# Kernel optimization log

Hardware: AMD Instinct MI355X
Metric: run time of the kernel (lower is better)

The kernel has to match this reference:

```python
import jax, jax.numpy as jnp
import numpy as np

T, D_MODEL, D_FF, N_EXPERTS, TOP_K = 8192, 1024, 4096, 8, 2

def setup_inputs() -> dict:
    key = jax.random.key(0)
    k1, k2, k3, k4, k5 = jax.random.split(key, 5)
    hidden_states = jax.random.normal(k1, (T, D_MODEL), dtype=jnp.float32)
    # router picks TOP_K distinct-ish experts per token; build one-hot mask [T, K, E]
    expert_idx = jax.random.randint(k2, (T, TOP_K), 0, N_EXPERTS)
    selected_experts = jax.nn.one_hot(expert_idx, N_EXPERTS, dtype=jnp.int32)
    rw = jax.random.uniform(k3, (T, TOP_K), dtype=jnp.float32)
    routing_weights = rw / jnp.sum(rw, axis=-1, keepdims=True)
    scale = 1.0 / np.sqrt(D_MODEL)
    wi = jax.random.normal(k4, (N_EXPERTS, D_FF, D_MODEL), dtype=jnp.float32) * scale
    wo = jax.random.normal(k5, (N_EXPERTS, D_MODEL, D_FF), dtype=jnp.float32) * (1.0 / np.sqrt(D_FF))
    return {"hidden_states": hidden_states, "selected_experts": selected_experts,
            "routing_weights": routing_weights, "wi": wi, "wo": wo}

def reference(hidden_states, selected_experts, routing_weights, wi, wo):
    # expert_mask: [E, K, T] (as in torch permute(2,1,0))
    mask = jnp.transpose(selected_experts, (2, 1, 0)).astype(hidden_states.dtype)
    # combined per-token weight for each expert: w[t, e] = sum_k mask[e,k,t]*routing_weights[t,k]
    w = jnp.einsum('ekt,tk->te', mask, routing_weights)
    out = jnp.zeros_like(hidden_states)
    # fixed small loop over experts; tokens not routed to expert e get weight 0,
    # so this is mathematically identical to the gather->MLP->scale->scatter-add.
    for e in range(wi.shape[0]):
        h = jax.nn.relu(hidden_states @ wi[e].T)     # [T, d_ff] (dropout is identity at eval)
        y = h @ wo[e].T                              # [T, d_model]
        out = out + w[:, e:e + 1] * y
    return out
```

## Files before the change

kernel.cpp:

```cpp
#include <hip/hip_runtime.h>
#include <hip/hip_bf16.h>


#define T_TOK   8192
#define D_MODEL 1024
#define D_FF    4096
#define NE      8
#define BM      128
#define BK      64
#define MT_MAX  136
#define ROWS_MAX (MT_MAX * 128)

typedef float f32x4 __attribute__((ext_vector_type(4)));
typedef short s16x8 __attribute__((ext_vector_type(8)));
typedef short s16x4 __attribute__((ext_vector_type(4)));
typedef unsigned short u16;

__device__ __forceinline__ u16 f2bf(float x) {
  __hip_bfloat16 h = __float2bfloat16(x);
  return *reinterpret_cast<u16*>(&h);
}

__device__ __forceinline__ s16x8 cvt8(float4 a, float4 b) {
  s16x8 v;
  v[0] = (short)f2bf(a.x); v[1] = (short)f2bf(a.y);
  v[2] = (short)f2bf(a.z); v[3] = (short)f2bf(a.w);
  v[4] = (short)f2bf(b.x); v[5] = (short)f2bf(b.y);
  v[6] = (short)f2bf(b.z); v[7] = (short)f2bf(b.w);
  return v;
}

__device__ __forceinline__ void gload_lds16(const void* g, void* l) {
  __builtin_amdgcn_global_load_lds((const __attribute__((address_space(1))) void*)g,
                                   (__attribute__((address_space(3))) void*)l,
                                   16, 0, 0);
}

__global__ void moe_route(const int* __restrict__ sel, const float* __restrict__ rw,
                          int* __restrict__ cnt, int* __restrict__ tidx,
                          float* __restrict__ tw) {
  int t = blockIdx.x * blockDim.x + threadIdx.x;
  if (t >= T_TOK) return;
  int e0 = 0, e1 = 0;
  #pragma unroll
  for (int e = 0; e < NE; ++e) {
    if (sel[t * 16 + e])     e0 = e;
    if (sel[t * 16 + 8 + e]) e1 = e;
  }
  float w0 = rw[2 * t], w1 = rw[2 * t + 1];
  if (e0 == e1) {
    int p = atomicAdd(&cnt[e0], 1);
    tidx[e0 * T_TOK + p] = t; tw[e0 * T_TOK + p] = w0 + w1;
  } else {
    int p = atomicAdd(&cnt[e0], 1);
    tidx[e0 * T_TOK + p] = t; tw[e0 * T_TOK + p] = w0;
    int q = atomicAdd(&cnt[e1], 1);
    tidx[e1 * T_TOK + q] = t; tw[e1 * T_TOK + q] = w1;
  }
}

__global__ void moe_tilemap(const int* __restrict__ cnt, const int* __restrict__ tidx,
                            const float* __restrict__ tw, int* __restrict__ tile_e,
                            int* __restrict__ tokr, float* __restrict__ wr) {
  int off[NE + 1];
  {
    int o = 0;
    #pragma unroll
    for (int e = 0; e < NE; ++e) { off[e] = o; o += (cnt[e] + 127) & ~127; }
    off[NE] = o;
  }
  const int total = off[NE];
  const int gid = blockIdx.x * blockDim.x + threadIdx.x;
  const int stride = gridDim.x * blockDim.x;
  for (int t = gid; t < MT_MAX; t += stride) {
    int r0 = t * 128; int e = -1;
    if (r0 < total) {
      #pragma unroll
      for (int i = NE - 1; i >= 0; --i) if (r0 >= off[i]) { e = i; break; }
    }
    tile_e[t] = e;
  }
  for (int i = gid; i < ROWS_MAX; i += stride) {
    if (i >= total) { tokr[i] = -1; wr[i] = 0.f; continue; }
    int e = 0;
    #pragma unroll
    for (int k = NE - 1; k >= 0; --k) if (i >= off[k]) { e = k; break; }
    int j = i - off[e];
    int ok = j < cnt[e];
    tokr[i] = ok ? tidx[e * T_TOK + j] : -1;
    wr[i]   = ok ? tw[e * T_TOK + j] : 0.f;
  }
}

__global__ void moe_gather_x(const float* __restrict__ hs, const int* __restrict__ tokr,
                             u16* __restrict__ Xg) {
  int row = blockIdx.x;
  int tok = tokr[row];
  int c = threadIdx.x * 4;
  u16* dst = Xg + (size_t)row * D_MODEL + c;
  s16x4 o;
  if (tok < 0) {
    o[0] = o[1] = o[2] = o[3] = 0;
  } else {
    float4 v = *(const float4*)(hs + (size_t)tok * D_MODEL + c);
    o[0] = (short)f2bf(v.x); o[1] = (short)f2bf(v.y);
    o[2] = (short)f2bf(v.z); o[3] = (short)f2bf(v.w);
  }
  *(s16x4*)dst = o;
}

__global__ void moe_cvt_w(const float* __restrict__ wi, const float* __restrict__ wo,
                          u16* __restrict__ wib, u16* __restrict__ wob) {
  const size_t NW = (size_t)NE * D_FF * D_MODEL;
  size_t i = ((size_t)blockIdx.x * blockDim.x + threadIdx.x) * 8;
  const float* src; u16* dst;
  if (i < NW) { src = wi + i; dst = wib + i; }
  else        { src = wo + (i - NW); dst = wob + (i - NW); }
  float4 a = *(const float4*)(src);
  float4 b = *(const float4*)(src + 4);
  *(s16x8*)dst = cvt8(a, b);
}

__global__ void moe_cvt_wi_s(const float* __restrict__ wi, u16* __restrict__ wis,
                             int W, int f0) {
  size_t i = ((size_t)blockIdx.x * blockDim.x + threadIdx.x) * 8;
  size_t per = (size_t)W * D_MODEL;
  int e = (int)(i / per); size_t r = i % per;
  const float* src = wi + ((size_t)e * D_FF + f0) * D_MODEL + r;
  float4 a = *(const float4*)src;
  float4 b = *(const float4*)(src + 4);
  *(s16x8*)(wis + i) = cvt8(a, b);
}

__global__ void moe_cvt_wo_s(const float* __restrict__ wo, u16* __restrict__ wos,
                             int W, int f0) {
  size_t i = ((size_t)blockIdx.x * blockDim.x + threadIdx.x) * 8;
  size_t per = (size_t)D_MODEL * W;
  int e = (int)(i / per); size_t r = i % per;
  int row = (int)(r / W), col = (int)(r % W);
  const float* src = wo + ((size_t)e * D_MODEL + row) * D_FF + f0 + col;
  float4 a = *(const float4*)src;
  float4 b = *(const float4*)(src + 4);
  *(s16x8*)(wos + i) = cvt8(a, b);
}

template <bool FULL>
__global__ __launch_bounds__(256, 4)
void moe_g1(const u16* __restrict__ Xg, const u16* __restrict__ wiP,
            const int* __restrict__ tile_e, u16* __restrict__ H,
            int W, int f0) {
  __shared__ u16 As[BM * BK];
  __shared__ u16 Bs[BM * BK];

  const int GR = gridDim.x;
  const int task = (blockIdx.x & 7) * (GR >> 3) + (blockIdx.x >> 3);
  const int mt = task % MT_MAX;
  const int nc = task / MT_MAX;
  const int e = tile_e[mt];
  if (e < 0) return;
  const int grow0 = mt * 128;
  const int fl = nc * 128;

  const int tid = threadIdx.x;
  const int lane = tid & 63, wv = tid >> 6;
  const int lg = lane >> 4, ll = lane & 15;
  const int wm = wv >> 1, wn = wv & 1;

  const u16* abase0 = Xg + (size_t)grow0 * D_MODEL;
  const u16* bbase0 = wiP + (FULL ? ((size_t)e * D_FF + f0 + fl)
                                  : ((size_t)e * W + fl)) * D_MODEL;

  f32x4 acc[4][4];
  #pragma unroll
  for (int m = 0; m < 4; ++m)
    #pragma unroll
    for (int n = 0; n < 4; ++n) acc[m][n] = (f32x4){0.f, 0.f, 0.f, 0.f};

  for (int kk = 0; kk < D_MODEL / BK; ++kk) {
    __syncthreads();
    const u16* ab = abase0 + kk * BK;
    #pragma unroll
    for (int i = 0; i < 4; ++i) {
      int off = wv * 4096 + i * 1024 + lane * 16;
      int row = off >> 7, colb = off & 127;
      gload_lds16(ab + (size_t)row * D_MODEL + (colb >> 1), (char*)As + off);
    }
    const u16* bb = bbase0 + kk * BK;
    #pragma unroll
    for (int i = 0; i < 4; ++i) {
      int off = wv * 4096 + i * 1024 + lane * 16;
      int row = off >> 7, colb = off & 127;
      gload_lds16(bb + (size_t)row * D_MODEL + (colb >> 1), (char*)Bs + off);
    }
    __syncthreads();
    #pragma unroll
    for (int kb = 0; kb < 2; ++kb) {
      s16x8 af[4], bf[4];
      #pragma unroll
      for (int m = 0; m < 4; ++m)
        af[m] = *(const s16x8*)(As + (wm * 64 + m * 16 + ll) * BK + kb * 32 + lg * 8);
      #pragma unroll
      for (int n = 0; n < 4; ++n)
        bf[n] = *(const s16x8*)(Bs + (wn * 64 + n * 16 + ll) * BK + kb * 32 + lg * 8);
      #pragma unroll
      for (int m = 0; m < 4; ++m)
        #pragma unroll
        for (int n = 0; n < 4; ++n)
          acc[m][n] = __builtin_amdgcn_mfma_f32_16x16x32_bf16(af[m], bf[n], acc[m][n], 0, 0, 0);
    }
  }

  const int hc = fl + wn * 64 + ll;
  #pragma unroll
  for (int m = 0; m < 4; ++m) {
    #pragma unroll
    for (int r = 0; r < 4; ++r) {
      int row = grow0 + wm * 64 + m * 16 + lg * 4 + r;
      u16* hp = H + (size_t)row * W + hc;
      #pragma unroll
      for (int n = 0; n < 4; ++n) {
        float v = acc[m][n][r];
        hp[n * 16] = f2bf(v > 0.f ? v : 0.f);
      }
    }
  }
}

template <bool FULL>
__global__ __launch_bounds__(256, 4)
void moe_g2(const u16* __restrict__ H, const u16* __restrict__ woP,
            const int* __restrict__ tile_e, const int* __restrict__ tokr,
            const float* __restrict__ wr, float* __restrict__ out,
            int W, int f0, int KCH) {
  __shared__ u16 As[BM * BK];
  __shared__ u16 Bs[BM * BK];
  __shared__ int s_tok[BM];
  __shared__ float s_w[BM];

  const int GR = gridDim.x;
  const int task = (blockIdx.x & 7) * (GR >> 3) + (blockIdx.x >> 3);
  const int dc = task & 7;
  const int rest = task >> 3;
  const int mt = rest % MT_MAX;
  const int kc = rest / MT_MAX;
  const int e = tile_e[mt];
  if (e < 0) return;
  const int grow0 = mt * 128;
  const int dcol0 = dc * 128;

  const int tid = threadIdx.x;
  const int lane = tid & 63, wv = tid >> 6;
  const int lg = lane >> 4, ll = lane & 15;
  const int wm = wv >> 1, wn = wv & 1;

  if (tid < BM) { s_tok[tid] = tokr[grow0 + tid]; s_w[tid] = wr[grow0 + tid]; }
  __syncthreads();

  const u16* abase0 = H + (size_t)grow0 * W + (size_t)kc * KCH;
  const size_t bpitch = FULL ? (size_t)D_FF : (size_t)W;
  const u16* bbase0 = woP + ((size_t)e * D_MODEL + dcol0) * bpitch
                      + (FULL ? f0 : 0) + (size_t)kc * KCH;

  f32x4 acc[4][4];
  #pragma unroll
  for (int m = 0; m < 4; ++m)
    #pragma unroll
    for (int n = 0; n < 4; ++n) acc[m][n] = (f32x4){0.f, 0.f, 0.f, 0.f};

  for (int kk = 0; kk < KCH / BK; ++kk) {
    __syncthreads();
    const u16* ab = abase0 + kk * BK;
    #pragma unroll
    for (int i = 0; i < 4; ++i) {
      int off = wv * 4096 + i * 1024 + lane * 16;
      int row = off >> 7, colb = off & 127;
      gload_lds16(ab + (size_t)row * W + (colb >> 1), (char*)As + off);
    }
    const u16* bb = bbase0 + kk * BK;
    #pragma unroll
    for (int i = 0; i < 4; ++i) {
      int off = wv * 4096 + i * 1024 + lane * 16;
      int row = off >> 7, colb = off & 127;
      gload_lds16(bb + (size_t)row * bpitch + (colb >> 1), (char*)Bs + off);
    }
    __syncthreads();
    #pragma unroll
    for (int kb = 0; kb < 2; ++kb) {
      s16x8 af[4], bf[4];
      #pragma unroll
      for (int m = 0; m < 4; ++m)
        af[m] = *(const s16x8*)(As + (wm * 64 + m * 16 + ll) * BK + kb * 32 + lg * 8);
      #pragma unroll
      for (int n = 0; n < 4; ++n)
        bf[n] = *(const s16x8*)(Bs + (wn * 64 + n * 16 + ll) * BK + kb * 32 + lg * 8);
      #pragma unroll
      for (int m = 0; m < 4; ++m)
        #pragma unroll
        for (int n = 0; n < 4; ++n)
          acc[m][n] = __builtin_amdgcn_mfma_f32_16x16x32_bf16(af[m], bf[n], acc[m][n], 0, 0, 0);
    }
  }

  #pragma unroll
  for (int m = 0; m < 4; ++m) {
    #pragma unroll
    for (int r = 0; r < 4; ++r) {
      int row = wm * 64 + m * 16 + lg * 4 + r;
      int tok = s_tok[row];
      if (tok >= 0) {
        float w = s_w[row];
        float* op = out + (size_t)tok * D_MODEL + dcol0 + wn * 64 + ll;
        #pragma unroll
        for (int n = 0; n < 4; ++n)
          atomicAdd(op + n * 16, acc[m][n][r] * w);
      }
    }
  }
}

extern "C" void kernel_launch(void* const* d_in, const int* in_sizes, int n_in,
                              void* d_out, int out_size, void* d_ws, size_t ws_size,
                              hipStream_t stream) {
  const float* hs  = (const float*)d_in[0];
  const int*   sel = (const int*)d_in[1];
  const float* rw  = (const float*)d_in[2];
  const float* wi  = (const float*)d_in[3];
  const float* wo  = (const float*)d_in[4];
  float* out = (float*)d_out;

  const size_t NW   = (size_t)NE * D_FF * D_MODEL;
  const size_t CTRL = 1u << 20;
  const size_t WB   = 2 * NW * sizeof(u16);
  const size_t XGB  = (size_t)ROWS_MAX * D_MODEL * 2;

  bool FULLW = true; int W = D_FF;
  {
    bool found = false;
    for (int f : {1, 2, 4, 8, 16}) {
      int Wc = D_FF / f;
      size_t need = CTRL + WB + XGB + (size_t)ROWS_MAX * Wc * 2;
      if (need <= ws_size) { FULLW = true; W = Wc; found = true; break; }
    }
    if (!found) {
      for (int Wc : {1024, 512, 256}) {
        size_t sl = (size_t)2 * NE * Wc * D_MODEL * 2;
        size_t need = CTRL + sl + XGB + (size_t)ROWS_MAX * Wc * 2;
        if (need <= ws_size) { FULLW = false; W = Wc; break; }
      }
    }
  }
  const int FS = D_FF / W;

  size_t off = 0;
  auto take = [&](size_t b) -> char* {
    char* r = (char*)d_ws + off; off = (off + b + 255) & ~(size_t)255; return r;
  };
  int*   tidx = (int*)take((size_t)NE * T_TOK * 4);
  float* tw   = (float*)take((size_t)NE * T_TOK * 4);
  int*   tokr = (int*)take((size_t)ROWS_MAX * 4);
  float* wrr  = (float*)take((size_t)ROWS_MAX * 4);
  int*   te   = (int*)take(MT_MAX * 4);
  int*   cnt  = (int*)take(256);
  off = CTRL;
  u16 *wiP, *woP;
  if (FULLW) { wiP = (u16*)take(NW * 2); woP = (u16*)take(NW * 2); }
  else       { wiP = (u16*)take((size_t)NE * W * D_MODEL * 2);
               woP = (u16*)take((size_t)NE * D_MODEL * W * 2); }
  u16* Xg   = (u16*)take(XGB);
  u16* Hbuf = (u16*)take((size_t)ROWS_MAX * W * 2);

  hipMemsetAsync(cnt, 0, 256, stream);
  hipMemsetAsync(d_out, 0, (size_t)out_size * sizeof(float), stream);
  moe_route<<<T_TOK / 256, 256, 0, stream>>>(sel, rw, cnt, tidx, tw);
  moe_tilemap<<<64, 256, 0, stream>>>(cnt, tidx, tw, te, tokr, wrr);
  moe_gather_x<<<ROWS_MAX, 256, 0, stream>>>(hs, tokr, Xg);
  if (FULLW)
    moe_cvt_w<<<(int)(2 * NW / 8 / 256), 256, 0, stream>>>(wi, wo, wiP, woP);

  const int KCH = (W >= 2048) ? 2048 : W;
  const int g1grid = MT_MAX * (W / 128);
  const int g2grid = MT_MAX * 8 * (W / KCH);
  const int cvtblk = (int)(((size_t)NE * W * D_MODEL / 8) / 256);

  for (int p = 0; p < FS; ++p) {
    const int f0 = p * W;
    if (!FULLW) {
      moe_cvt_wi_s<<<cvtblk, 256, 0, stream>>>(wi, wiP, W, f0);
      moe_cvt_wo_s<<<cvtblk, 256, 0, stream>>>(wo, woP, W, f0);
    }
    if (FULLW) {
      moe_g1<true><<<g1grid, 256, 0, stream>>>(Xg, wiP, te, Hbuf, W, f0);
      moe_g2<true><<<g2grid, 256, 0, stream>>>(Hbuf, woP, te, tokr, wrr, out, W, f0, KCH);
    } else {
      moe_g1<false><<<g1grid, 256, 0, stream>>>(Xg, wiP, te, Hbuf, W, f0);
      moe_g2<false><<<g2grid, 256, 0, stream>>>(Hbuf, woP, te, tokr, wrr, out, W, f0, KCH);
    }
  }
}
```

Before: 571.7 us.

## Rewrite first expert GEMM with 256x256 tiles and triple-buffered LDS pipeline

The first grouped GEMM (X·Wi with ReLU) now runs 512-thread blocks computing 256x256 output tiles. It uses a three-stage dynamic-LDS ring with manual vmcnt waits, XOR-swizzled LDS layout and setprio around MFMA bursts. Expert segments are padded to 256 rows so that larger tiles stay within a single expert, and a second tile-to-expert map is kept for the unchanged 128-row second GEMM. This aims to raise data reuse and hide global load latency, at the cost of more padding rows, lower occupancy (one block per CU) and more careful synchronisation.

```diff
diff --git a/kernel.cpp b/kernel.cpp
--- a/kernel.cpp
+++ b/kernel.cpp
@@ -8,8 +8,11 @@
 #define NE      8
 #define BM      128
 #define BK      64
-#define MT_MAX  136
-#define ROWS_MAX (MT_MAX * 128)
+#define MT2     72
+#define MT_MAX  (MT2 * 2)
+#define ROWS_MAX (MT2 * 256)
+#define BUFB    32768
+#define LDS_G1  98304
 
 typedef float f32x4 __attribute__((ext_vector_type(4)));
 typedef short s16x8 __attribute__((ext_vector_type(8)));
@@ -60,13 +63,14 @@
 }
 
 __global__ void moe_tilemap(const int* __restrict__ cnt, const int* __restrict__ tidx,
-                            const float* __restrict__ tw, int* __restrict__ tile_e,
-                            int* __restrict__ tokr, float* __restrict__ wr) {
+                            const float* __restrict__ tw, int* __restrict__ te128,
+                            int* __restrict__ te256, int* __restrict__ tokr,
+                            float* __restrict__ wr) {
   int off[NE + 1];
   {
     int o = 0;
     #pragma unroll
-    for (int e = 0; e < NE; ++e) { off[e] = o; o += (cnt[e] + 127) & ~127; }
+    for (int e = 0; e < NE; ++e) { off[e] = o; o += (cnt[e] + 255) & ~255; }
     off[NE] = o;
   }
   const int total = off[NE];
@@ -78,7 +82,8 @@
       #pragma unroll
       for (int i = NE - 1; i >= 0; --i) if (r0 >= off[i]) { e = i; break; }
     }
-    tile_e[t] = e;
+    te128[t] = e;
+    if ((t & 1) == 0) te256[t >> 1] = e;
   }
   for (int i = gid; i < ROWS_MAX; i += stride) {
     if (i >= total) { tokr[i] = -1; wr[i] = 0.f; continue; }
@@ -145,30 +150,169 @@
 }
 
 template <bool FULL>
+__global__ __launch_bounds__(512, 1)
+void moe_g1(const u16* __restrict__ Xg, const u16* __restrict__ wiP,
+            const int* __restrict__ te256, u16* __restrict__ H,
+            int W, int f0) {
+  extern __shared__ char lds[];
+  const int GR = gridDim.x;
+  const int task = (blockIdx.x & 7) * (GR >> 3) + (blockIdx.x >> 3);
+  const int mt = task % MT2;
+  const int nc = task / MT2;
+  const int e = te256[mt];
+  if (e < 0) return;
+  const int grow0 = mt * 256;
+  const int fcol = nc * 256;
+
+  const int tid = threadIdx.x;
+  const int lane = tid & 63, wv = tid >> 6;
+  const int lg = lane >> 4, ll = lane & 15;
+  const int wm = wv >> 2, wn = wv & 3;
+
+  const int sw = (tid * 16) ^ (((tid >> 3) & 7) << 4);
+  const int srow = sw >> 6, scol = sw & 63;
+  const int inner = (ll * 64 + lg * 16) ^ (((ll >> 1) & 7) << 4);
+
+  const char* gA = (const char*)(Xg + (size_t)grow0 * D_MODEL);
+  const char* gB = (const char*)(wiP + (FULL ? ((size_t)e * D_FF + f0 + fcol)
+                                             : ((size_t)e * W + fcol)) * D_MODEL);
+
+  f32x4 acc[8][4];
+  #pragma unroll
+  for (int m = 0; m < 8; ++m)
+    #pragma unroll
+    for (int n = 0; n < 4; ++n) acc[m][n] = (f32x4){0.f, 0.f, 0.f, 0.f};
+
+  auto stage = [&](int kb, char* lbuf) {
+    #pragma unroll
+    for (int j = 0; j < 2; ++j)
+      gload_lds16(gA + (size_t)(j * 128 + srow) * 2048 + kb + scol,
+                  lbuf + j * 8192 + tid * 16);
+    #pragma unroll
+    for (int j = 0; j < 2; ++j)
+      gload_lds16(gB + (size_t)(j * 128 + srow) * 2048 + kb + scol,
+                  lbuf + 16384 + j * 8192 + tid * 16);
+  };
+
+  const int NT = D_MODEL / 32;
+  stage(0, lds);
+  stage(64, lds + BUFB);
+  int bufi = 0;
+  for (int t = 0; t < NT; ++t) {
+    if (t < NT - 1) { asm volatile("s_waitcnt vmcnt(4)" ::: "memory"); }
+    else            { asm volatile("s_waitcnt vmcnt(0)" ::: "memory"); }
+    asm volatile("s_barrier" ::: "memory");
+    const char* la = lds + bufi * BUFB + wm * 8192;
+    const char* lb = lds + bufi * BUFB + 16384 + wn * 4096;
+    if (t + 2 < NT) {
+      int b2 = bufi + 2; if (b2 >= 3) b2 -= 3;
+      stage((t + 2) * 64, lds + b2 * BUFB);
+    }
+    s16x8 bq0 = *(const s16x8*)(lb + 0 * 1024 + inner);
+    s16x8 bq1 = *(const s16x8*)(lb + 1 * 1024 + inner);
+    s16x8 bq2 = *(const s16x8*)(lb + 2 * 1024 + inner);
+    s16x8 bq3 = *(const s16x8*)(lb + 3 * 1024 + inner);
+    {
+      s16x8 a0 = *(const s16x8*)(la + 0 * 1024 + inner);
+      s16x8 a1 = *(const s16x8*)(la + 1 * 1024 + inner);
+      s16x8 a2 = *(const s16x8*)(la + 2 * 1024 + inner);
+      s16x8 a3 = *(const s16x8*)(la + 3 * 1024 + inner);
+      __builtin_amdgcn_s_setprio(1);
+      acc[0][0] = __builtin_amdgcn_mfma_f32_16x16x32_bf16(a0, bq0, acc[0][0], 0, 0, 0);
+      acc[0][1] = __builtin_amdgcn_mfma_f32_16x16x32_bf16(a0, bq1, acc[0][1], 0, 0, 0);
+      acc[0][2] = __builtin_amdgcn_mfma_f32_16x16x32_bf16(a0, bq2, acc[0][2], 0, 0, 0);
+      acc[0][3] = __builtin_amdgcn_mfma_f32_16x16x32_bf16(a0, bq3, acc[0][3], 0, 0, 0);
+      acc[1][0] = __builtin_amdgcn_mfma_f32_16x16x32_bf16(a1, bq0, acc[1][0], 0, 0, 0);
+      acc[1][1] = __builtin_amdgcn_mfma_f32_16x16x32_bf16(a1, bq1, acc[1][1], 0, 0, 0);
+      acc[1][2] = __builtin_amdgcn_mfma_f32_16x16x32_bf16(a1, bq2, acc[1][2], 0, 0, 0);
+      acc[1][3] = __builtin_amdgcn_mfma_f32_16x16x32_bf16(a1, bq3, acc[1][3], 0, 0, 0);
+      acc[2][0] = __builtin_amdgcn_mfma_f32_16x16x32_bf16(a2, bq0, acc[2][0], 0, 0, 0);
+      acc[2][1] = __builtin_amdgcn_mfma_f32_16x16x32_bf16(a2, bq1, acc[2][1], 0, 0, 0);
+      acc[2][2] = __builtin_amdgcn_mfma_f32_16x16x32_bf16(a2, bq2, acc[2][2], 0, 0, 0);
+      acc[2][3] = __builtin_amdgcn_mfma_f32_16x16x32_bf16(a2, bq3, acc[2][3], 0, 0, 0);
+      acc[3][0] = __builtin_amdgcn_mfma_f32_16x16x32_bf16(a3, bq0, acc[3][0], 0, 0, 0);
+      acc[3][1] = __builtin_amdgcn_mfma_f32_16x16x32_bf16(a3, bq1, acc[3][1], 0, 0, 0);
+      acc[3][2] = __builtin_amdgcn_mfma_f32_16x16x32_bf16(a3, bq2, acc[3][2], 0, 0, 0);
+      acc[3][3] = __builtin_amdgcn_mfma_f32_16x16x32_bf16(a3, bq3, acc[3][3], 0, 0, 0);
+      __builtin_amdgcn_s_setprio(0);
+    }
+    __builtin_amdgcn_s_barrier();
+    {
+      s16x8 a0 = *(const s16x8*)(la + 4 * 1024 + inner);
+      s16x8 a1 = *(const s16x8*)(la + 5 * 1024 + inner);
+      s16x8 a2 = *(const s16x8*)(la + 6 * 1024 + inner);
+      s16x8 a3 = *(const s16x8*)(la + 7 * 1024 + inner);
+      __builtin_amdgcn_s_setprio(1);
+      acc[4][0] = __builtin_amdgcn_mfma_f32_16x16x32_bf16(a0, bq0, acc[4][0], 0, 0, 0);
+      acc[4][1] = __builtin_amdgcn_mfma_f32_16x16x32_bf16(a0, bq1, acc[4][1], 0, 0, 0);
+      acc[4][2] = __builtin_amdgcn_mfma_f32_16x16x32_bf16(a0, bq2, acc[4][2], 0, 0, 0);
+      acc[4][3] = __builtin_amdgcn_mfma_f32_16x16x32_bf16(a0, bq3, acc[4][3], 0, 0, 0);
+      acc[5][0] = __builtin_amdgcn_mfma_f32_16x16x32_bf16(a1, bq0, acc[5][0], 0, 0, 0);
+      acc[5][1] = __builtin_amdgcn_mfma_f32_16x16x32_bf16(a1, bq1, acc[5][1], 0, 0, 0);
+      acc[5][2] = __builtin_amdgcn_mfma_f32_16x16x32_bf16(a1, bq2, acc[5][2], 0, 0, 0);
+      acc[5][3] = __builtin_amdgcn_mfma_f32_16x16x32_bf16(a1, bq3, acc[5][3], 0, 0, 0);
+      acc[6][0] = __builtin_amdgcn_mfma_f32_16x16x32_bf16(a2, bq0, acc[6][0], 0, 0, 0);
+      acc[6][1] = __builtin_amdgcn_mfma_f32_16x16x32_bf16(a2, bq1, acc[6][1], 0, 0, 0);
+      acc[6][2] = __builtin_amdgcn_mfma_f32_16x16x32_bf16(a2, bq2, acc[6][2], 0, 0, 0);
+      acc[6][3] = __builtin_amdgcn_mfma_f32_16x16x32_bf16(a2, bq3, acc[6][3], 0, 0, 0);
+      acc[7][0] = __builtin_amdgcn_mfma_f32_16x16x32_bf16(a3, bq0, acc[7][0], 0, 0, 0);
+      acc[7][1] = __builtin_amdgcn_mfma_f32_16x16x32_bf16(a3, bq1, acc[7][1], 0, 0, 0);
+      acc[7][2] = __builtin_amdgcn_mfma_f32_16x16x32_bf16(a3, bq2, acc[7][2], 0, 0, 0);
+      acc[7][3] = __builtin_amdgcn_mfma_f32_16x16x32_bf16(a3, bq3, acc[7][3], 0, 0, 0);
+      __builtin_amdgcn_s_setprio(0);
+    }
+    bufi += 1; if (bufi >= 3) bufi -= 3;
+  }
+
+  #pragma unroll
+  for (int mf = 0; mf < 8; ++mf) {
+    #pragma unroll
+    for (int r = 0; r < 4; ++r) {
+      int row = grow0 + wm * 128 + mf * 16 + lg * 4 + r;
+      u16* hp = H + (size_t)row * W + fcol + wn * 64 + ll;
+      #pragma unroll
+      for (int nf = 0; nf < 4; ++nf) {
+        float v = acc[mf][nf][r];
+        hp[nf * 16] = f2bf(v > 0.f ? v : 0.f);
+      }
+    }
+  }
+}
+
+template <bool FULL>
 __global__ __launch_bounds__(256, 4)
-void moe_g1(const u16* __restrict__ Xg, const u16* __restrict__ wiP,
-            const int* __restrict__ tile_e, u16* __restrict__ H,
-            int W, int f0) {
+void moe_g2(const u16* __restrict__ H, const u16* __restrict__ woP,
+            const int* __restrict__ te128, const int* __restrict__ tokr,
+            const float* __restrict__ wr, float* __restrict__ out,
+            int W, int f0, int KCH) {
   __shared__ u16 As[BM * BK];
   __shared__ u16 Bs[BM * BK];
+  __shared__ int s_tok[BM];
+  __shared__ float s_w[BM];
 
   const int GR = gridDim.x;
   const int task = (blockIdx.x & 7) * (GR >> 3) + (blockIdx.x >> 3);
-  const int mt = task % MT_MAX;
-  const int nc = task / MT_MAX;
-  const int e = tile_e[mt];
+  const int dc = task & 7;
+  const int rest = task >> 3;
+  const int mt = rest % MT_MAX;
+  const int kc = rest / MT_MAX;
+  const int e = te128[mt];
   if (e < 0) return;
   const int grow0 = mt * 128;
-  const int fl = nc * 128;
+  const int dcol0 = dc * 128;
 
   const int tid = threadIdx.x;
   const int lane = tid & 63, wv = tid >> 6;
   const int lg = lane >> 4, ll = lane & 15;
   const int wm = wv >> 1, wn = wv & 1;
 
-  const u16* abase0 = Xg + (size_t)grow0 * D_MODEL;
-  const u16* bbase0 = wiP + (FULL ? ((size_t)e * D_FF + f0 + fl)
-                                  : ((size_t)e * W + fl)) * D_MODEL;
+  if (tid < BM) { s_tok[tid] = tokr[grow0 + tid]; s_w[tid] = wr[grow0 + tid]; }
+  __syncthreads();
+
+  const u16* abase0 = H + (size_t)grow0 * W + (size_t)kc * KCH;
+  const size_t bpitch = FULL ? (size_t)D_FF : (size_t)W;
+  const u16* bbase0 = woP + ((size_t)e * D_MODEL + dcol0) * bpitch
+                      + (FULL ? f0 : 0) + (size_t)kc * KCH;
 
   f32x4 acc[4][4];
   #pragma unroll
@@ -176,21 +320,21 @@
     #pragma unroll
     for (int n = 0; n < 4; ++n) acc[m][n] = (f32x4){0.f, 0.f, 0.f, 0.f};
 
-  for (int kk = 0; kk < D_MODEL / BK; ++kk) {
+  for (int kk = 0; kk < KCH / BK; ++kk) {
     __syncthreads();
     const u16* ab = abase0 + kk * BK;
     #pragma unroll
     for (int i = 0; i < 4; ++i) {
       int off = wv * 4096 + i * 1024 + lane * 16;
       int row = off >> 7, colb = off & 127;
-      gload_lds16(ab + (size_t)row * D_MODEL + (colb >> 1), (char*)As + off);
+      gload_lds16(ab + (size_t)row * W + (colb >> 1), (char*)As + off);
     }
     const u16* bb = bbase0 + kk * BK;
     #pragma unroll
     for (int i = 0; i < 4; ++i) {
       int off = wv * 4096 + i * 1024 + lane * 16;
       int row = off >> 7, colb = off & 127;
-      gload_lds16(bb + (size_t)row * D_MODEL + (colb >> 1), (char*)Bs + off);
+      gload_lds16(bb + (size_t)row * bpitch + (colb >> 1), (char*)Bs + off);
     }
     __syncthreads();
     #pragma unroll
@@ -210,97 +354,6 @@
     }
   }
 
-  const int hc = fl + wn * 64 + ll;
-  #pragma unroll
-  for (int m = 0; m < 4; ++m) {
-    #pragma unroll
-    for (int r = 0; r < 4; ++r) {
-      int row = grow0 + wm * 64 + m * 16 + lg * 4 + r;
-      u16* hp = H + (size_t)row * W + hc;
-      #pragma unroll
-      for (int n = 0; n < 4; ++n) {
-        float v = acc[m][n][r];
-        hp[n * 16] = f2bf(v > 0.f ? v : 0.f);
-      }
-    }
-  }
-}
-
-template <bool FULL>
-__global__ __launch_bounds__(256, 4)
-void moe_g2(const u16* __restrict__ H, const u16* __restrict__ woP,
-            const int* __restrict__ tile_e, const int* __restrict__ tokr,
-            const float* __restrict__ wr, float* __restrict__ out,
-            int W, int f0, int KCH) {
-  __shared__ u16 As[BM * BK];
-  __shared__ u16 Bs[BM * BK];
-  __shared__ int s_tok[BM];
-  __shared__ float s_w[BM];
-
-  const int GR = gridDim.x;
-  const int task = (blockIdx.x & 7) * (GR >> 3) + (blockIdx.x >> 3);
-  const int dc = task & 7;
-  const int rest = task >> 3;
-  const int mt = rest % MT_MAX;
-  const int kc = rest / MT_MAX;
-  const int e = tile_e[mt];
-  if (e < 0) return;
-  const int grow0 = mt * 128;
-  const int dcol0 = dc * 128;
-
-  const int tid = threadIdx.x;
-  const int lane = tid & 63, wv = tid >> 6;
-  const int lg = lane >> 4, ll = lane & 15;
-  const int wm = wv >> 1, wn = wv & 1;
-
-  if (tid < BM) { s_tok[tid] = tokr[grow0 + tid]; s_w[tid] = wr[grow0 + tid]; }
-  __syncthreads();
-
-  const u16* abase0 = H + (size_t)grow0 * W + (size_t)kc * KCH;
-  const size_t bpitch = FULL ? (size_t)D_FF : (size_t)W;
-  const u16* bbase0 = woP + ((size_t)e * D_MODEL + dcol0) * bpitch
-                      + (FULL ? f0 : 0) + (size_t)kc * KCH;
-
-  f32x4 acc[4][4];
-  #pragma unroll
-  for (int m = 0; m < 4; ++m)
-    #pragma unroll
-    for (int n = 0; n < 4; ++n) acc[m][n] = (f32x4){0.f, 0.f, 0.f, 0.f};
-
-  for (int kk = 0; kk < KCH / BK; ++kk) {
-    __syncthreads();
-    const u16* ab = abase0 + kk * BK;
-    #pragma unroll
-    for (int i = 0; i < 4; ++i) {
-      int off = wv * 4096 + i * 1024 + lane * 16;
-      int row = off >> 7, colb = off & 127;
-      gload_lds16(ab + (size_t)row * W + (colb >> 1), (char*)As + off);
-    }
-    const u16* bb = bbase0 + kk * BK;
-    #pragma unroll
-    for (int i = 0; i < 4; ++i) {
-      int off = wv * 4096 + i * 1024 + lane * 16;
-      int row = off >> 7, colb = off & 127;
-      gload_lds16(bb + (size_t)row * bpitch + (colb >> 1), (char*)Bs + off);
-    }
-    __syncthreads();
-    #pragma unroll
-    for (int kb = 0; kb < 2; ++kb) {
-      s16x8 af[4], bf[4];
-      #pragma unroll
-      for (int m = 0; m < 4; ++m)
-        af[m] = *(const s16x8*)(As + (wm * 64 + m * 16 + ll) * BK + kb * 32 + lg * 8);
-      #pragma unroll
-      for (int n = 0; n < 4; ++n)
-        bf[n] = *(const s16x8*)(Bs + (wn * 64 + n * 16 + ll) * BK + kb * 32 + lg * 8);
-      #pragma unroll
-      for (int m = 0; m < 4; ++m)
-        #pragma unroll
-        for (int n = 0; n < 4; ++n)
-          acc[m][n] = __builtin_amdgcn_mfma_f32_16x16x32_bf16(af[m], bf[n], acc[m][n], 0, 0, 0);
-    }
-  }
-
   #pragma unroll
   for (int m = 0; m < 4; ++m) {
     #pragma unroll
@@ -360,6 +413,7 @@
   int*   tokr = (int*)take((size_t)ROWS_MAX * 4);
   float* wrr  = (float*)take((size_t)ROWS_MAX * 4);
   int*   te   = (int*)take(MT_MAX * 4);
+  int*   te2  = (int*)take(MT2 * 4);
   int*   cnt  = (int*)take(256);
   off = CTRL;
   u16 *wiP, *woP;
@@ -372,13 +426,18 @@
   hipMemsetAsync(cnt, 0, 256, stream);
   hipMemsetAsync(d_out, 0, (size_t)out_size * sizeof(float), stream);
   moe_route<<<T_TOK / 256, 256, 0, stream>>>(sel, rw, cnt, tidx, tw);
-  moe_tilemap<<<64, 256, 0, stream>>>(cnt, tidx, tw, te, tokr, wrr);
+  moe_tilemap<<<64, 256, 0, stream>>>(cnt, tidx, tw, te, te2, tokr, wrr);
   moe_gather_x<<<ROWS_MAX, 256, 0, stream>>>(hs, tokr, Xg);
   if (FULLW)
     moe_cvt_w<<<(int)(2 * NW / 8 / 256), 256, 0, stream>>>(wi, wo, wiP, woP);
 
+  hipFuncSetAttribute(reinterpret_cast<const void*>(&moe_g1<true>),
+                      hipFuncAttributeMaxDynamicSharedMemorySize, LDS_G1);
+  hipFuncSetAttribute(reinterpret_cast<const void*>(&moe_g1<false>),
+                      hipFuncAttributeMaxDynamicSharedMemorySize, LDS_G1);
+
   const int KCH = (W >= 2048) ? 2048 : W;
-  const int g1grid = MT_MAX * (W / 128);
+  const int g1grid = MT2 * (W / 256);
   const int g2grid = MT_MAX * 8 * (W / KCH);
   const int cvtblk = (int)(((size_t)NE * W * D_MODEL / 8) / 256);
 
@@ -389,10 +448,10 @@
       moe_cvt_wo_s<<<cvtblk, 256, 0, stream>>>(wo, woP, W, f0);
     }
     if (FULLW) {
-      moe_g1<true><<<g1grid, 256, 0, stream>>>(Xg, wiP, te, Hbuf, W, f0);
+      moe_g1<true><<<g1grid, 512, LDS_G1, stream>>>(Xg, wiP, te2, Hbuf, W, f0);
       moe_g2<true><<<g2grid, 256, 0, stream>>>(Hbuf, woP, te, tokr, wrr, out, W, f0, KCH);
     } else {
-      moe_g1<false><<<g1grid, 256, 0, stream>>>(Xg, wiP, te, Hbuf, W, f0);
+      moe_g1<false><<<g1grid, 512, LDS_G1, stream>>>(Xg, wiP, te2, Hbuf, W, f0);
       moe_g2<false><<<g2grid, 256, 0, stream>>>(Hbuf, woP, te, tokr, wrr, out, W, f0, KCH);
     }
   }
```

Result: faster. 549.0 us (-4.0%).
